# Kernel tuning notes

Measured on AMD Instinct MI355X. Metric: run time of the kernel, lower is better.

Reference implementation:

```python
import jax, jax.numpy as jnp
import numpy as np

B, N, D, H, DEG = 2, 20000, 256, 8, 8
E = N * DEG
EPS = 1e-3  # keras LayerNormalization default epsilon


def layer_norm(x, gamma, beta):
    mu = jnp.mean(x, axis=-1, keepdims=True)
    var = jnp.mean(jnp.square(x - mu), axis=-1, keepdims=True)
    return (x - mu) * jax.lax.rsqrt(var + EPS) * gamma + beta


def setup_inputs() -> dict:
    key = jax.random.key(0)
    ks = jax.random.split(key, 8)
    x = jax.random.normal(ks[0], (B, N, D), dtype=jnp.float32)
    # edge list sorted by source node; every node has DEG out-edges so
    # segment_sum covers all N segments (matches tf.math.segment_sum semantics)
    src = jnp.repeat(jnp.arange(N, dtype=jnp.int64), DEG)
    dst = jax.random.randint(ks[1], (E,), 0, N, dtype=jnp.int64)
    edges = jnp.stack([src, dst], axis=1)  # [E, 2]
    scale = 0.05
    wq = jax.random.normal(ks[2], (D, D), dtype=jnp.float32) * scale
    wk = jax.random.normal(ks[3], (D, D), dtype=jnp.float32) * scale
    wv = jax.random.normal(ks[4], (D, D), dtype=jnp.float32) * scale
    wo = jax.random.normal(ks[5], (D, D), dtype=jnp.float32) * scale
    zeros = jnp.zeros((D,), dtype=jnp.float32)
    ones = jnp.ones((D,), dtype=jnp.float32)
    return {
        "x": x, "edges": edges,
        "wq": wq, "bq": zeros, "wk": wk, "bk": zeros,
        "wv": wv, "bv": zeros, "wo": wo, "bo": zeros,
        "gamma1": ones, "beta1": zeros, "gamma2": ones, "beta2": zeros,
    }


def reference(x, edges, wq, bq, wk, bk, wv, bv, wo, bo, gamma1, beta1, gamma2, beta2):
    b, n, d = x.shape
    h, dh = H, D // H
    xn = layer_norm(x, gamma1, beta1)                      # [B,N,D]
    # QKV projections, split heads, move node axis to front: [N,B,H,dh]
    def proj(w, bias):
        y = (xn @ w + bias).reshape(b, n, h, dh)
        return jnp.transpose(y, (1, 0, 2, 3))
    q, k, v = proj(wq, bq), proj(wk, bk), proj(wv, bv)
    src, dst = edges[:, 0], edges[:, 1]
    q_part = q[src]                                         # [E,B,H,dh]
    k_part = k[dst]
    v_part = v[dst]
    logits = jnp.sum(q_part * k_part, axis=-1, keepdims=True) / jnp.sqrt(
        jnp.asarray(dh, dtype=x.dtype))                     # [E,B,H,1]
    w = jnp.exp(logits)                                     # unnormalized softmax (as in source)
    num = jax.ops.segment_sum(v_part * w, src, num_segments=n)  # [N,B,H,dh]
    den = jax.ops.segment_sum(w, src, num_segments=n)           # [N,B,H,1]
    attn = num / den
    attn = jnp.transpose(attn, (1, 0, 2, 3)).reshape(b, n, d)   # [B,N,D]
    concat = xn + attn                                      # residual uses normed input (source reassigns `inputs`)
    out = layer_norm(concat, gamma2, beta2)
    out = jax.nn.relu(out @ wo + bo)
    return out + concat
```

## Files before the change

### kernel.cpp

```cpp
#include <hip/hip_runtime.h>


typedef __bf16 bf16x8 __attribute__((ext_vector_type(8)));
typedef float  f32x4  __attribute__((ext_vector_type(4)));

__device__ __forceinline__ float bf2f(unsigned short u) {
    union { unsigned int i; float f; } v; v.i = ((unsigned int)u) << 16; return v.f;
}
__device__ __forceinline__ unsigned short f2bf(float f) {
    union { float f; unsigned int i; } v; v.f = f;
    unsigned int x = v.i;
    unsigned int r = (x + 0x7FFFu + ((x >> 16) & 1u)) >> 16;
    return (unsigned short)r;
}

#define NNODE 20000
#define ROWS  40000
#define DMODEL 256

__global__ __launch_bounds__(256) void prep_ln1_kernel(
    const float* __restrict__ wq, const float* __restrict__ wk,
    const float* __restrict__ wv, const float* __restrict__ wo,
    const float* __restrict__ bq, const float* __restrict__ bk,
    const float* __restrict__ bv, const float* __restrict__ bo,
    const float* __restrict__ x,
    const float* __restrict__ g1, const float* __restrict__ b1,
    unsigned short* __restrict__ Wqkvt,
    unsigned short* __restrict__ Wot,
    float* __restrict__ biasq,
    float* __restrict__ biaso,
    unsigned short* __restrict__ xn)
{
    if (blockIdx.x < 1024) {
        int idx = blockIdx.x * 256 + threadIdx.x;
        if (idx < 768 * 256) {
            int n = idx >> 8, k = idx & 255;
            int sel = n >> 8, nl = n & 255;
            const float* w = (sel == 0) ? wq : (sel == 1) ? wk : wv;
            Wqkvt[idx] = f2bf(w[k * 256 + nl]);
        } else {
            int idx2 = idx - 768 * 256;
            int n = idx2 >> 8, k = idx2 & 255;
            Wot[idx2] = f2bf(wo[k * 256 + n]);
        }
        if (idx < 768) {
            const float* bb = (idx < 256) ? bq : (idx < 512) ? bk : bv;
            biasq[idx] = bb[idx & 255];
        }
        if (idx >= 768 && idx < 1024) biaso[idx - 768] = bo[idx - 768];
        return;
    }
    int wave = threadIdx.x >> 6, lane = threadIdx.x & 63;
    int sub = lane >> 5, hl = lane & 31;
    int m = (blockIdx.x - 1024) * 8 + wave * 2 + sub;
    const float* xp = x + (size_t)m * DMODEL + hl * 8;
    float4 x0 = *(const float4*)xp;
    float4 x1 = *(const float4*)(xp + 4);
    float f[8] = {x0.x, x0.y, x0.z, x0.w, x1.x, x1.y, x1.z, x1.w};
    float s = 0.f, ss = 0.f;
    #pragma unroll
    for (int t = 0; t < 8; ++t) { s += f[t]; ss += f[t]*f[t]; }
    #pragma unroll
    for (int mk = 1; mk < 32; mk <<= 1) { s += __shfl_xor(s, mk); ss += __shfl_xor(ss, mk); }
    float mu  = s * (1.f/256.f);
    float var = ss * (1.f/256.f) - mu*mu;
    float rs  = rsqrtf(var + 1e-3f);
    float4 g0 = *(const float4*)(g1 + hl * 8);
    float4 g1v = *(const float4*)(g1 + hl * 8 + 4);
    float4 b0 = *(const float4*)(b1 + hl * 8);
    float4 b1v = *(const float4*)(b1 + hl * 8 + 4);
    float gg[8] = {g0.x, g0.y, g0.z, g0.w, g1v.x, g1v.y, g1v.z, g1v.w};
    float bb[8] = {b0.x, b0.y, b0.z, b0.w, b1v.x, b1v.y, b1v.z, b1v.w};
    unsigned short o[8];
    #pragma unroll
    for (int t = 0; t < 8; ++t) o[t] = f2bf((f[t] - mu) * rs * gg[t] + bb[t]);
    *(int4*)(xn + (size_t)m * DMODEL + hl * 8) = *(const int4*)o;
}

#define LDSW 264
#define MFMA_BF16(d, a, b) d = __builtin_amdgcn_mfma_f32_16x16x32_bf16(a, b, d, 0, 0, 0)

template<bool EPI>
__global__ __launch_bounds__(512, 1) void gemm_kernel(
    const unsigned short* __restrict__ A,
    const unsigned short* __restrict__ Bt,
    const float* __restrict__ bias,
    void* __restrict__ C,
    const unsigned short* __restrict__ resid,
    int M, int Ncols)
{
    __shared__ unsigned short As[128 * LDSW];
    __shared__ unsigned short Bs[128 * LDSW];
    int tid  = threadIdx.x;
    int wave = tid >> 6, lane = tid & 63;
    int quad = lane >> 4, l16 = lane & 15;

    int nt_total = Ncols >> 7;
    int nwg = gridDim.x;
    int xcd = blockIdx.x & 7, loc = blockIdx.x >> 3;
    int qq = nwg >> 3, rr = nwg & 7;
    int wid = (xcd < rr) ? (xcd * (qq + 1) + loc)
                         : (rr * (qq + 1) + (xcd - rr) * qq + loc);
    int mt = wid / nt_total;
    int nt = wid - mt * nt_total;
    int m0 = mt * 128, n0 = nt * 128;
    int wm = (wave >> 1) * 32, wn = (wave & 1) * 64;

    int srow = tid >> 2;
    int c16  = (tid & 3) * 16;
    int arow = m0 + srow; if (arow >= M) arow = M - 1;
    const unsigned short* Ap = A  + (size_t)arow * 256 + c16;
    const unsigned short* Bp = Bt + (size_t)(n0 + srow) * 256 + c16;
    unsigned short* AsP = &As[srow * LDSW + c16];
    unsigned short* BsP = &Bs[srow * LDSW + c16];
    #pragma unroll
    for (int j = 0; j < 4; ++j) {
        int4 a0 = *(const int4*)(Ap + j * 64);
        int4 a1 = *(const int4*)(Ap + j * 64 + 8);
        int4 b0 = *(const int4*)(Bp + j * 64);
        int4 b1 = *(const int4*)(Bp + j * 64 + 8);
        *(int4*)(AsP + j * 64)     = a0;
        *(int4*)(AsP + j * 64 + 8) = a1;
        *(int4*)(BsP + j * 64)     = b0;
        *(int4*)(BsP + j * 64 + 8) = b1;
    }
    __syncthreads();

    f32x4 acc00 = {}, acc01 = {}, acc02 = {}, acc03 = {};
    f32x4 acc10 = {}, acc11 = {}, acc12 = {}, acc13 = {};

    #pragma unroll
    for (int ks = 0; ks < 256; ks += 32) {
        int ca = ks + quad * 8;
        bf16x8 a0 = *(const bf16x8*)&As[(wm +  0 + l16) * LDSW + ca];
        bf16x8 a1 = *(const bf16x8*)&As[(wm + 16 + l16) * LDSW + ca];
        bf16x8 b0 = *(const bf16x8*)&Bs[(wn +  0 + l16) * LDSW + ca];
        bf16x8 b1 = *(const bf16x8*)&Bs[(wn + 16 + l16) * LDSW + ca];
        bf16x8 b2 = *(const bf16x8*)&Bs[(wn + 32 + l16) * LDSW + ca];
        bf16x8 b3 = *(const bf16x8*)&Bs[(wn + 48 + l16) * LDSW + ca];
        MFMA_BF16(acc00, a0, b0); MFMA_BF16(acc01, a0, b1);
        MFMA_BF16(acc02, a0, b2); MFMA_BF16(acc03, a0, b3);
        MFMA_BF16(acc10, a1, b0); MFMA_BF16(acc11, a1, b1);
        MFMA_BF16(acc12, a1, b2); MFMA_BF16(acc13, a1, b3);
    }

#define EPI_STORE(accv, R, CC) do {                                          \
        int col = n0 + wn + (CC) * 16 + l16;                                 \
        float bb = bias[col];                                                \
        int rowb = m0 + wm + (R) * 16 + quad * 4;                            \
        _Pragma("unroll")                                                    \
        for (int rr = 0; rr < 4; ++rr) {                                     \
            int row = rowb + rr;                                             \
            if (row < M) {                                                   \
                float v = (accv)[rr] + bb;                                   \
                if (EPI) {                                                   \
                    v = fmaxf(v, 0.f);                                       \
                    v += bf2f(resid[(size_t)row * 256 + col]);               \
                    ((float*)C)[(size_t)row * Ncols + col] = v;              \
                } else {                                                     \
                    ((unsigned short*)C)[(size_t)row * Ncols + col] = f2bf(v);\
                }                                                            \
            }                                                                \
        }                                                                    \
    } while (0)

    EPI_STORE(acc00, 0, 0); EPI_STORE(acc01, 0, 1); EPI_STORE(acc02, 0, 2); EPI_STORE(acc03, 0, 3);
    EPI_STORE(acc10, 1, 0); EPI_STORE(acc11, 1, 1); EPI_STORE(acc12, 1, 2); EPI_STORE(acc13, 1, 3);
#undef EPI_STORE
}

__global__ __launch_bounds__(1024) void attn_kernel(
    const unsigned short* __restrict__ qkv,
    const int* __restrict__ edges,
    const unsigned short* __restrict__ xn,
    const float* __restrict__ g2, const float* __restrict__ b2,
    unsigned short* __restrict__ concat,
    unsigned short* __restrict__ h2)
{
    int wave = threadIdx.x >> 6, lane = threadIdx.x & 63;
    int i = blockIdx.x * 16 + wave;
    int b = lane >> 5, hl = lane & 31;
    size_t m = (size_t)b * NNODE + i;

    int jv = 0;
    if (lane < 8) jv = edges[2 * (i * 8 + lane) + 1];

    int4 qi = *(const int4*)(qkv + m * 768 + hl * 8);
    int4 xi = *(const int4*)(xn + m * DMODEL + hl * 8);
    const unsigned short* qs = (const unsigned short*)&qi;
    float qf[8];
    #pragma unroll
    for (int t = 0; t < 8; ++t) qf[t] = bf2f(qs[t]);

#define KVLOAD(E)                                                                  \
    int j##E = __shfl(jv, E);                                                      \
    const unsigned short* kp##E = qkv + ((size_t)b * NNODE + j##E) * 768 + 256 + hl * 8; \
    int4 KI##E = *(const int4*)(kp##E);                                            \
    int4 VI##E = *(const int4*)(kp##E + 256);
    KVLOAD(0) KVLOAD(1) KVLOAD(2) KVLOAD(3)
    KVLOAD(4) KVLOAD(5) KVLOAD(6) KVLOAD(7)
#undef KVLOAD

    float acc[8] = {};
    float den = 0.f;
    const float scale = 0.17677669529663687f;
#define EDGE(E) do {                                                         \
        const unsigned short* ks = (const unsigned short*)&KI##E;            \
        const unsigned short* vs = (const unsigned short*)&VI##E;            \
        float dot = 0.f;                                                     \
        _Pragma("unroll")                                                    \
        for (int t = 0; t < 8; ++t) dot += qf[t] * bf2f(ks[t]);              \
        dot += __shfl_xor(dot, 1);                                           \
        dot += __shfl_xor(dot, 2);               \
        float w = __expf(dot * scale);                                       \
        _Pragma("unroll")                                                    \
        for (int t = 0; t < 8; ++t) acc[t] += w * bf2f(vs[t]);               \
        den += w;                                                            \
    } while (0)
    EDGE(0); EDGE(1); EDGE(2); EDGE(3);
    EDGE(4); EDGE(5); EDGE(6); EDGE(7);
#undef EDGE
    float inv = 1.f / den;

    const unsigned short* xs = (const unsigned short*)&xi;
    float c[8], s = 0.f, ss = 0.f;
    #pragma unroll
    for (int t = 0; t < 8; ++t) { c[t] = bf2f(xs[t]) + acc[t] * inv; s += c[t]; ss += c[t]*c[t]; }
    #pragma unroll
    for (int mk = 1; mk < 32; mk <<= 1) { s += __shfl_xor(s, mk); ss += __shfl_xor(ss, mk); }
    float mu  = s * (1.f/256.f);
    float var = ss * (1.f/256.f) - mu*mu;
    float rs  = rsqrtf(var + 1e-3f);

    float4 ga = *(const float4*)(g2 + hl * 8);
    float4 gb = *(const float4*)(g2 + hl * 8 + 4);
    float4 ba = *(const float4*)(b2 + hl * 8);
    float4 bb = *(const float4*)(b2 + hl * 8 + 4);
    float gg[8] = {ga.x, ga.y, ga.z, ga.w, gb.x, gb.y, gb.z, gb.w};
    float bv[8] = {ba.x, ba.y, ba.z, ba.w, bb.x, bb.y, bb.z, bb.w};
    unsigned short oc[8], oh[8];
    #pragma unroll
    for (int t = 0; t < 8; ++t) {
        oc[t] = f2bf(c[t]);
        oh[t] = f2bf((c[t] - mu) * rs * gg[t] + bv[t]);
    }
    *(int4*)(concat + m * DMODEL + hl * 8) = *(const int4*)oc;
    *(int4*)(h2     + m * DMODEL + hl * 8) = *(const int4*)oh;
}

extern "C" void kernel_launch(void* const* d_in, const int* in_sizes, int n_in,
                              void* d_out, int out_size, void* d_ws, size_t ws_size,
                              hipStream_t stream)
{
    const float* x   = (const float*)d_in[0];
    const int* edges = (const int*)d_in[1];
    const float* wq = (const float*)d_in[2];
    const float* bq = (const float*)d_in[3];
    const float* wk = (const float*)d_in[4];
    const float* bk = (const float*)d_in[5];
    const float* wv = (const float*)d_in[6];
    const float* bv = (const float*)d_in[7];
    const float* wo = (const float*)d_in[8];
    const float* bo = (const float*)d_in[9];
    const float* g1 = (const float*)d_in[10];
    const float* b1 = (const float*)d_in[11];
    const float* g2 = (const float*)d_in[12];
    const float* b2 = (const float*)d_in[13];

    char* ws = (char*)d_ws;
    unsigned short* Wqkvt = (unsigned short*)(ws);
    unsigned short* Wot   = (unsigned short*)(ws + 393216);
    float* biasq          = (float*)(ws + 393216 + 131072);
    float* biaso          = (float*)(ws + 393216 + 131072 + 3072);
    size_t off = 393216 + 131072 + 4096;
    unsigned short* xn     = (unsigned short*)(ws + off); off += (size_t)ROWS * DMODEL * 2;
    unsigned short* qkv    = (unsigned short*)(ws + off); off += (size_t)ROWS * 768 * 2;
    unsigned short* concat = (unsigned short*)(ws + off); off += (size_t)ROWS * DMODEL * 2;
    unsigned short* h2     = (unsigned short*)(ws + off); off += (size_t)ROWS * DMODEL * 2;

    prep_ln1_kernel<<<1024 + ROWS / 8, 256, 0, stream>>>(
        wq, wk, wv, wo, bq, bk, bv, bo, x, g1, b1, Wqkvt, Wot, biasq, biaso, xn);
    gemm_kernel<false><<<dim3(313 * 6), 512, 0, stream>>>(xn, Wqkvt, biasq, qkv, nullptr, ROWS, 768);
    attn_kernel<<<NNODE / 16, 1024, 0, stream>>>(qkv, edges, xn, g2, b2, concat, h2);
    gemm_kernel<true><<<dim3(313 * 2), 512, 0, stream>>>(h2, Wot, biaso, d_out, concat, ROWS, 256);
}
```

Baseline: 247.8 us.

## Double-buffer GEMM K-tiles in LDS and allow two workgroups per CU

The GEMM no longer loads the full 256-wide K slab into LDS at once. It now streams K in 64-wide chunks through two LDS buffers with register staging, so global loads of the next chunk overlap MFMA compute on the current one. LDS use drops from about 135KB to about 73KB, and launch bounds now allow two 512-thread workgroups per CU for better occupancy. The cost is more barriers and extra registers for the staged tiles, which could limit the occupancy gain.

```diff
diff --git a/kernel.cpp b/kernel.cpp
--- a/kernel.cpp
+++ b/kernel.cpp
@@ -77,11 +77,12 @@
     *(int4*)(xn + (size_t)m * DMODEL + hl * 8) = *(const int4*)o;
 }
 
-#define LDSW 264
+#define LDS_W 72
+#define BUFSZ (128 * LDS_W)
 #define MFMA_BF16(d, a, b) d = __builtin_amdgcn_mfma_f32_16x16x32_bf16(a, b, d, 0, 0, 0)
 
 template<bool EPI>
-__global__ __launch_bounds__(512, 1) void gemm_kernel(
+__global__ __launch_bounds__(512, 2) void gemm_kernel(
     const unsigned short* __restrict__ A,
     const unsigned short* __restrict__ Bt,
     const float* __restrict__ bias,
@@ -89,8 +90,8 @@
     const unsigned short* __restrict__ resid,
     int M, int Ncols)
 {
-    __shared__ unsigned short As[128 * LDSW];
-    __shared__ unsigned short Bs[128 * LDSW];
+    __shared__ unsigned short As[2 * BUFSZ];
+    __shared__ unsigned short Bs[2 * BUFSZ];
     int tid  = threadIdx.x;
     int wave = tid >> 6, lane = tid & 63;
     int quad = lane >> 4, l16 = lane & 15;
@@ -107,42 +108,72 @@
     int wm = (wave >> 1) * 32, wn = (wave & 1) * 64;
 
     int srow = tid >> 2;
-    int c16  = (tid & 3) * 16;
+    int scol = (tid & 3) * 16;
     int arow = m0 + srow; if (arow >= M) arow = M - 1;
-    const unsigned short* Ap = A  + (size_t)arow * 256 + c16;
-    const unsigned short* Bp = Bt + (size_t)(n0 + srow) * 256 + c16;
-    unsigned short* AsP = &As[srow * LDSW + c16];
-    unsigned short* BsP = &Bs[srow * LDSW + c16];
-    #pragma unroll
-    for (int j = 0; j < 4; ++j) {
-        int4 a0 = *(const int4*)(Ap + j * 64);
-        int4 a1 = *(const int4*)(Ap + j * 64 + 8);
-        int4 b0 = *(const int4*)(Bp + j * 64);
-        int4 b1 = *(const int4*)(Bp + j * 64 + 8);
-        *(int4*)(AsP + j * 64)     = a0;
-        *(int4*)(AsP + j * 64 + 8) = a1;
-        *(int4*)(BsP + j * 64)     = b0;
-        *(int4*)(BsP + j * 64 + 8) = b1;
-    }
-    __syncthreads();
+    const unsigned short* Ap = A  + (size_t)arow * 256 + scol;
+    const unsigned short* Bp = Bt + (size_t)(n0 + srow) * 256 + scol;
+    unsigned short* AsP = &As[srow * LDS_W + scol];
+    unsigned short* BsP = &Bs[srow * LDS_W + scol];
 
     f32x4 acc00 = {}, acc01 = {}, acc02 = {}, acc03 = {};
     f32x4 acc10 = {}, acc11 = {}, acc12 = {}, acc13 = {};
 
-    #pragma unroll
-    for (int ks = 0; ks < 256; ks += 32) {
-        int ca = ks + quad * 8;
-        bf16x8 a0 = *(const bf16x8*)&As[(wm +  0 + l16) * LDSW + ca];
-        bf16x8 a1 = *(const bf16x8*)&As[(wm + 16 + l16) * LDSW + ca];
-        bf16x8 b0 = *(const bf16x8*)&Bs[(wn +  0 + l16) * LDSW + ca];
-        bf16x8 b1 = *(const bf16x8*)&Bs[(wn + 16 + l16) * LDSW + ca];
-        bf16x8 b2 = *(const bf16x8*)&Bs[(wn + 32 + l16) * LDSW + ca];
-        bf16x8 b3 = *(const bf16x8*)&Bs[(wn + 48 + l16) * LDSW + ca];
-        MFMA_BF16(acc00, a0, b0); MFMA_BF16(acc01, a0, b1);
-        MFMA_BF16(acc02, a0, b2); MFMA_BF16(acc03, a0, b3);
-        MFMA_BF16(acc10, a1, b0); MFMA_BF16(acc11, a1, b1);
-        MFMA_BF16(acc12, a1, b2); MFMA_BF16(acc13, a1, b3);
-    }
+    int4 s0a0, s0a1, s0b0, s0b1;
+    int4 s1a0, s1a1, s1b0, s1b1;
+
+#define STAGE_LOAD(S, KT) do {                         \
+        S##a0 = *(const int4*)(Ap + (KT) * 64);        \
+        S##a1 = *(const int4*)(Ap + (KT) * 64 + 8);    \
+        S##b0 = *(const int4*)(Bp + (KT) * 64);        \
+        S##b1 = *(const int4*)(Bp + (KT) * 64 + 8);    \
+    } while (0)
+#define STAGE_WRITE(S, BUF) do {                       \
+        *(int4*)(AsP + (BUF) * BUFSZ)     = S##a0;     \
+        *(int4*)(AsP + (BUF) * BUFSZ + 8) = S##a1;     \
+        *(int4*)(BsP + (BUF) * BUFSZ)     = S##b0;     \
+        *(int4*)(BsP + (BUF) * BUFSZ + 8) = S##b1;     \
+    } while (0)
+#define COMPUTE(BUF) do {                                                          \
+        _Pragma("unroll")                                                          \
+        for (int ks = 0; ks < 64; ks += 32) {                                      \
+            int ca = (BUF) * BUFSZ + ks + quad * 8;                                \
+            bf16x8 a0 = *(const bf16x8*)&As[ca + (wm +  0 + l16) * LDS_W];         \
+            bf16x8 a1 = *(const bf16x8*)&As[ca + (wm + 16 + l16) * LDS_W];         \
+            bf16x8 b0 = *(const bf16x8*)&Bs[ca + (wn +  0 + l16) * LDS_W];         \
+            bf16x8 b1 = *(const bf16x8*)&Bs[ca + (wn + 16 + l16) * LDS_W];         \
+            bf16x8 b2 = *(const bf16x8*)&Bs[ca + (wn + 32 + l16) * LDS_W];         \
+            bf16x8 b3 = *(const bf16x8*)&Bs[ca + (wn + 48 + l16) * LDS_W];         \
+            MFMA_BF16(acc00, a0, b0); MFMA_BF16(acc01, a0, b1);                    \
+            MFMA_BF16(acc02, a0, b2); MFMA_BF16(acc03, a0, b3);                    \
+            MFMA_BF16(acc10, a1, b0); MFMA_BF16(acc11, a1, b1);                    \
+            MFMA_BF16(acc12, a1, b2); MFMA_BF16(acc13, a1, b3);                    \
+        }                                                                          \
+    } while (0)
+
+    STAGE_LOAD(s0, 0);
+    STAGE_LOAD(s1, 1);
+    STAGE_WRITE(s0, 0);
+    __syncthreads();
+
+    STAGE_LOAD(s0, 2);
+    COMPUTE(0);
+    STAGE_WRITE(s1, 1);
+    __syncthreads();
+
+    STAGE_LOAD(s1, 3);
+    COMPUTE(1);
+    STAGE_WRITE(s0, 0);
+    __syncthreads();
+
+    COMPUTE(0);
+    STAGE_WRITE(s1, 1);
+    __syncthreads();
+
+    COMPUTE(1);
+
+#undef STAGE_LOAD
+#undef STAGE_WRITE
+#undef COMPUTE
 
 #define EPI_STORE(accv, R, CC) do {                                          \
         int col = n0 + wn + (CC) * 16 + l16;                                 \
```

Measured after the change: 225.7 us. -8.9%, faster.
